# Kernel optimization log

Measured on AMD Instinct MI355X. Metric: run time of the kernel, lower is better.

Reference implementation:

```python
import jax, jax.numpy as jnp
import numpy as np

N_NODES = 50000
N_EDGES = 800000
IN_CH = 128
HID = 256
N_GRAPHS = 512


def setup_inputs() -> dict:
    key = jax.random.key(0)
    ks = jax.random.split(key, 10)
    x = jax.random.normal(ks[0], (N_NODES, IN_CH), dtype=jnp.float32)
    edge_index = jax.random.randint(ks[1], (2, N_EDGES), 0, N_NODES, dtype=jnp.int32)
    batch = jnp.sort(jax.random.randint(ks[2], (N_NODES,), 0, N_GRAPHS, dtype=jnp.int32))
    # GCNConv params (glorot-ish init)
    W0 = jax.random.normal(ks[3], (IN_CH, HID), dtype=jnp.float32) / np.sqrt(IN_CH)
    b0 = jnp.zeros((HID,), dtype=jnp.float32)
    W1 = jax.random.normal(ks[4], (HID, HID), dtype=jnp.float32) / np.sqrt(HID)
    b1 = jnp.zeros((HID,), dtype=jnp.float32)
    W2 = jax.random.normal(ks[5], (HID, HID), dtype=jnp.float32) / np.sqrt(HID)
    b2 = jnp.zeros((HID,), dtype=jnp.float32)
    return {"x": x, "W0": W0, "b0": b0, "W1": W1, "b1": b1, "W2": W2, "b2": b2,
            "edge_index": edge_index, "batch": batch}


def _gcn_norm(edge_index, num_nodes):
    # PyG gcn_norm with add_self_loops=True: A_hat = A + I, norm = D^-1/2 A_hat D^-1/2
    src, dst = edge_index[0], edge_index[1]
    loop = jnp.arange(num_nodes, dtype=src.dtype)
    src = jnp.concatenate([src, loop])
    dst = jnp.concatenate([dst, loop])
    deg = jax.ops.segment_sum(jnp.ones_like(dst, dtype=jnp.float32), dst,
                              num_segments=num_nodes)
    dinv = jnp.where(deg > 0, jax.lax.rsqrt(deg), 0.0)
    norm = dinv[src] * dinv[dst]  # [E + N]
    return src, dst, norm


def _gcn_conv(x, W, b, src, dst, norm, num_nodes):
    h = x @ W                                  # [N, out]
    msg = norm[:, None] * h[src]               # gather + scale, [E+N, out]
    out = jax.ops.segment_sum(msg, dst, num_segments=num_nodes)  # scatter-add
    return out + b


def reference(x, W0, b0, W1, b1, W2, b2, edge_index, batch):
    n = x.shape[0]
    src, dst, norm = _gcn_norm(edge_index, n)  # normalization is layer-independent
    h = jax.nn.relu(_gcn_conv(x, W0, b0, src, dst, norm, n))
    h = jax.nn.relu(_gcn_conv(h, W1, b1, src, dst, norm, n))
    h = jax.nn.relu(_gcn_conv(h, W2, b2, src, dst, norm, n))
    # global_add_pool: segment-sum node features by graph id
    return jax.ops.segment_sum(h, batch, num_segments=N_GRAPHS)
```

## Files before the change

kernel.cpp:

```cpp
#include <hip/hip_runtime.h>

constexpr int NN  = 50000;
constexpr int NE  = 800000;
constexpr int CIN = 128;
constexpr int CH  = 256;
constexpr int NG  = 512;

typedef unsigned short ushort_t;
typedef unsigned int uint_t;

static __device__ __forceinline__ ushort_t f2bf(float f) {
    uint_t u = __float_as_uint(f);
    u += 0x7fffu + ((u >> 16) & 1u);
    return (ushort_t)(u >> 16);
}

__global__ void conv_x_kernel(const float4* __restrict__ x, ushort4* __restrict__ xb, int n4) {
    int i = blockIdx.x * blockDim.x + threadIdx.x;
    if (i >= n4) return;
    float4 v = x[i];
    ushort4 o;
    o.x = f2bf(v.x); o.y = f2bf(v.y); o.z = f2bf(v.z); o.w = f2bf(v.w);
    xb[i] = o;
}

__global__ void conv_wt_kernel(const float* __restrict__ W, ushort_t* __restrict__ Wt, int K, int N) {
    int i = blockIdx.x * blockDim.x + threadIdx.x;
    if (i >= K * N) return;
    int k = i / N, n = i % N;
    Wt[(size_t)n * K + k] = f2bf(W[i]);
}

__global__ void count_kernel(const int* __restrict__ dst, int* __restrict__ cnt, int E) {
    int e = blockIdx.x * blockDim.x + threadIdx.x;
    if (e < E) atomicAdd(&cnt[dst[e]], 1);
}

__global__ __launch_bounds__(256) void scan_bsum_kernel(const int* __restrict__ cnt,
                                                        int* __restrict__ bsum, int n) {
    int i = blockIdx.x * 256 + threadIdx.x;
    int v = (i < n) ? cnt[i] : 0;
    #pragma unroll
    for (int off = 32; off >= 1; off >>= 1) v += __shfl_xor(v, off, 64);
    __shared__ int ws[4];
    if ((threadIdx.x & 63) == 0) ws[threadIdx.x >> 6] = v;
    __syncthreads();
    if (threadIdx.x == 0) bsum[blockIdx.x] = ws[0] + ws[1] + ws[2] + ws[3];
}

__global__ __launch_bounds__(256) void scan_boff_kernel(int* __restrict__ bsum, int nb) {
    int tid = threadIdx.x, lane = tid & 63, wid = tid >> 6;
    int v = (tid < nb) ? bsum[tid] : 0;
    int s = v;
    #pragma unroll
    for (int off = 1; off < 64; off <<= 1) {
        int t = __shfl_up(s, off, 64);
        if (lane >= off) s += t;
    }
    __shared__ int wsum[4];
    if (lane == 63) wsum[wid] = s;
    __syncthreads();
    int wadd = 0;
    #pragma unroll
    for (int w = 0; w < 4; w++) if (w < wid) wadd += wsum[w];
    if (tid < nb) bsum[tid] = wadd + s - v;
}

__global__ __launch_bounds__(256) void scan_final_kernel(const int* __restrict__ cnt,
                                                         const int* __restrict__ boff,
                                                         int* __restrict__ rowptr,
                                                         float* __restrict__ dinv, int n) {
    int tid = threadIdx.x, lane = tid & 63, wid = tid >> 6;
    int i = blockIdx.x * 256 + tid;
    int v = (i < n) ? cnt[i] : 0;
    int s = v;
    #pragma unroll
    for (int off = 1; off < 64; off <<= 1) {
        int t = __shfl_up(s, off, 64);
        if (lane >= off) s += t;
    }
    __shared__ int wsum[4];
    if (lane == 63) wsum[wid] = s;
    __syncthreads();
    int wadd = boff[blockIdx.x];
    #pragma unroll
    for (int w = 0; w < 4; w++) if (w < wid) wadd += wsum[w];
    if (i < n) {
        rowptr[i] = wadd + s - v;
        dinv[i]   = rsqrtf((float)v + 1.0f);
        if (i == n - 1) rowptr[n] = wadd + s;
    }
}

__global__ void scatter_kernel(const int* __restrict__ src, const int* __restrict__ dst,
                               const int* __restrict__ rowptr, int* __restrict__ cursor,
                               const float* __restrict__ dinv, int2* __restrict__ epack, int E) {
    int e = blockIdx.x * blockDim.x + threadIdx.x;
    if (e >= E) return;
    int d = dst[e];
    int s = src[e];
    int p = rowptr[d] + atomicAdd(&cursor[d], 1);
    epack[p] = make_int2(s, __float_as_int(dinv[s]));
}

template <int C, int MODE>
__global__ __launch_bounds__(256) void node_agg_kernel(
    const ushort_t* __restrict__ h, const int* __restrict__ rowptr,
    const int2* __restrict__ epack, const float* __restrict__ dinv,
    const float* __restrict__ bias, const int* __restrict__ batch,
    void* __restrict__ out_v, int n) {
    constexpr int V = C / 64;
    int wave = threadIdx.x >> 6;
    int lane = threadIdx.x & 63;
    int d = blockIdx.x * 4 + wave;
    if (d >= n) return;

    int beg = rowptr[d], end = rowptr[d + 1];
    float acc[V] = {};

    for (int e = beg; e < end; e += 8) {
        int   srcs[8];
        float wts[8];
        #pragma unroll
        for (int u = 0; u < 8; u++) {
            int idx = e + u;
            int2 ep = epack[min(idx, NE - 1)];
            bool a = idx < end;
            srcs[u] = a ? ep.x : d;
            wts[u]  = a ? __int_as_float(ep.y) : 0.0f;
        }
        if constexpr (V == 4) {
            uint_t ra[8], rb[8];
            #pragma unroll
            for (int u = 0; u < 8; u++) {
                const uint_t* row = (const uint_t*)(h + (size_t)srcs[u] * C);
                ra[u] = row[lane];
                rb[u] = row[64 + lane];
            }
            #pragma unroll
            for (int u = 0; u < 8; u++) {
                float w = wts[u];
                acc[0] += w * __uint_as_float(ra[u] << 16);
                acc[1] += w * __uint_as_float(ra[u] & 0xffff0000u);
                acc[2] += w * __uint_as_float(rb[u] << 16);
                acc[3] += w * __uint_as_float(rb[u] & 0xffff0000u);
            }
        } else {
            uint_t rv[8];
            #pragma unroll
            for (int u = 0; u < 8; u++)
                rv[u] = ((const uint_t*)(h + (size_t)srcs[u] * C))[lane];
            #pragma unroll
            for (int u = 0; u < 8; u++) {
                float w = wts[u];
                acc[0] += w * __uint_as_float(rv[u] << 16);
                acc[1] += w * __uint_as_float(rv[u] & 0xffff0000u);
            }
        }
    }

    float dd = dinv[d];
    float self[V];
    {
        const uint_t* row = (const uint_t*)(h + (size_t)d * C);
        uint_t sa = row[lane];
        self[0] = __uint_as_float(sa << 16);
        self[1] = __uint_as_float(sa & 0xffff0000u);
        if constexpr (V == 4) {
            uint_t sb = row[64 + lane];
            self[2] = __uint_as_float(sb << 16);
            self[3] = __uint_as_float(sb & 0xffff0000u);
        }
    }

    float r[V];
    if constexpr (MODE >= 1) {
        float2 bA = *(const float2*)(bias + 2 * lane);
        r[0] = fmaxf(dd * acc[0] + dd * dd * self[0] + bA.x, 0.0f);
        r[1] = fmaxf(dd * acc[1] + dd * dd * self[1] + bA.y, 0.0f);
        if constexpr (V == 4) {
            float2 bB = *(const float2*)(bias + 128 + 2 * lane);
            r[2] = fmaxf(dd * acc[2] + dd * dd * self[2] + bB.x, 0.0f);
            r[3] = fmaxf(dd * acc[3] + dd * dd * self[3] + bB.y, 0.0f);
        }
    } else {
        #pragma unroll
        for (int i = 0; i < V; i++)
            r[i] = dd * acc[i] + dd * dd * self[i];
    }

    if constexpr (MODE == 2) {
        float* o = (float*)out_v + (size_t)batch[d] * C;
        atomicAdd(o + 2 * lane, r[0]);
        atomicAdd(o + 2 * lane + 1, r[1]);
        if constexpr (V == 4) {
            atomicAdd(o + 128 + 2 * lane, r[2]);
            atomicAdd(o + 128 + 2 * lane + 1, r[3]);
        }
    } else {
        uint_t* o = (uint_t*)((ushort_t*)out_v + (size_t)d * C);
        o[lane] = (uint_t)f2bf(r[0]) | ((uint_t)f2bf(r[1]) << 16);
        if constexpr (V == 4)
            o[64 + lane] = (uint_t)f2bf(r[2]) | ((uint_t)f2bf(r[3]) << 16);
    }
}

typedef __attribute__((ext_vector_type(8))) short bf16x8;
typedef __attribute__((ext_vector_type(4))) float f32x4;

template <int MODE>
__global__ __launch_bounds__(256) void gemm_bf16_kernel(
    const ushort_t* __restrict__ A, const ushort_t* __restrict__ Wt,
    const float* __restrict__ bias, ushort_t* __restrict__ C, int M, int K) {
    __shared__ ushort_t As[128][40];
    __shared__ ushort_t Bs[128][40];
    int tid = threadIdx.x;
    int row0 = blockIdx.x * 128, col0 = blockIdx.y * 128;
    int lr = tid >> 2, lq = tid & 3;
    int lane = tid & 63, wv = tid >> 6;
    int wr = (wv >> 1) * 64, wc = (wv & 1) * 64;
    int r16 = lane & 15, quad = lane >> 4;

    f32x4 acc[4][4] = {};

    for (int k0 = 0; k0 < K; k0 += 32) {
        {
            int gr0 = row0 + lr, gr1 = row0 + lr + 64;
            uint4 a0 = make_uint4(0, 0, 0, 0), a1 = make_uint4(0, 0, 0, 0);
            if (gr0 < M) a0 = *(const uint4*)(A + (size_t)gr0 * K + k0 + lq * 8);
            if (gr1 < M) a1 = *(const uint4*)(A + (size_t)gr1 * K + k0 + lq * 8);
            *(uint4*)&As[lr][lq * 8]      = a0;
            *(uint4*)&As[lr + 64][lq * 8] = a1;
            uint4 b0 = *(const uint4*)(Wt + (size_t)(col0 + lr) * K + k0 + lq * 8);
            uint4 b1 = *(const uint4*)(Wt + (size_t)(col0 + lr + 64) * K + k0 + lq * 8);
            *(uint4*)&Bs[lr][lq * 8]      = b0;
            *(uint4*)&Bs[lr + 64][lq * 8] = b1;
        }
        __syncthreads();
        bf16x8 af[4], bfr[4];
        #pragma unroll
        for (int i = 0; i < 4; i++) af[i]  = *(const bf16x8*)&As[wr + i * 16 + r16][quad * 8];
        #pragma unroll
        for (int j = 0; j < 4; j++) bfr[j] = *(const bf16x8*)&Bs[wc + j * 16 + r16][quad * 8];
        #pragma unroll
        for (int i = 0; i < 4; i++)
            #pragma unroll
            for (int j = 0; j < 4; j++)
                acc[i][j] = __builtin_amdgcn_mfma_f32_16x16x32_bf16(af[i], bfr[j], acc[i][j], 0, 0, 0);
        __syncthreads();
    }

    #pragma unroll
    for (int j = 0; j < 4; j++) {
        int colc = col0 + wc + j * 16 + r16;
        float bval = (MODE == 1) ? bias[colc] : 0.0f;
        #pragma unroll
        for (int i = 0; i < 4; i++) {
            #pragma unroll
            for (int r = 0; r < 4; r++) {
                int row = row0 + wr + i * 16 + quad * 4 + r;
                if (row < M) {
                    float v = acc[i][j][r];
                    if (MODE == 1) v = fmaxf(v + bval, 0.0f);
                    C[(size_t)row * 256 + colc] = f2bf(v);
                }
            }
        }
    }
}

extern "C" void kernel_launch(void* const* d_in, const int* in_sizes, int n_in,
                              void* d_out, int out_size, void* d_ws, size_t ws_size,
                              hipStream_t stream) {
    const float* x   = (const float*)d_in[0];
    const float* W0  = (const float*)d_in[1];
    const float* b0  = (const float*)d_in[2];
    const float* W1  = (const float*)d_in[3];
    const float* b1  = (const float*)d_in[4];
    const float* W2  = (const float*)d_in[5];
    const float* b2  = (const float*)d_in[6];
    const int*   ei  = (const int*)d_in[7];
    const int*   src = ei;
    const int*   dst = ei + NE;
    const int*   batch = (const int*)d_in[8];
    float* out = (float*)d_out;

    char* ws = (char*)d_ws;
    ushort_t* Abf = (ushort_t*)ws;
    ushort_t* Bbf = (ushort_t*)(ws + 25600000ull);
    ushort_t* xbf = (ushort_t*)(ws + 51200000ull);
    ushort_t* W0t = (ushort_t*)(ws + 64000000ull);
    ushort_t* W1t = (ushort_t*)(ws + 64065536ull);
    ushort_t* W2t = (ushort_t*)(ws + 64196608ull);
    float*    dinv   = (float*)(ws + 64327680ull);
    int*      rowptr = (int*)  (ws + 64527680ull);
    int*      cnt    = (int*)  (ws + 64727808ull);
    int2*     epack  = (int2*) (ws + 64927808ull);
    int*      bsum   = (int*)  (ws + 71327808ull);

    const int scanBlocks = (NN + 255) / 256;
    const int nodeBlocks = (NN + 3) / 4;
    const dim3 ggrid((NN + 127) / 128, 2);

    conv_x_kernel<<<(NN * CIN / 4 + 255) / 256, 256, 0, stream>>>((const float4*)x, (ushort4*)xbf, NN * CIN / 4);
    conv_wt_kernel<<<(CIN * CH + 255) / 256, 256, 0, stream>>>(W0, W0t, CIN, CH);
    conv_wt_kernel<<<(CH * CH + 255) / 256, 256, 0, stream>>>(W1, W1t, CH, CH);
    conv_wt_kernel<<<(CH * CH + 255) / 256, 256, 0, stream>>>(W2, W2t, CH, CH);

    hipMemsetAsync(cnt, 0, (size_t)NN * 4, stream);
    count_kernel<<<(NE + 255) / 256, 256, 0, stream>>>(dst, cnt, NE);
    scan_bsum_kernel<<<scanBlocks, 256, 0, stream>>>(cnt, bsum, NN);
    scan_boff_kernel<<<1, 256, 0, stream>>>(bsum, scanBlocks);
    scan_final_kernel<<<scanBlocks, 256, 0, stream>>>(cnt, bsum, rowptr, dinv, NN);
    hipMemsetAsync(cnt, 0, (size_t)NN * 4, stream);
    scatter_kernel<<<(NE + 255) / 256, 256, 0, stream>>>(src, dst, rowptr, cnt, dinv, epack, NE);

    node_agg_kernel<CIN, 0><<<nodeBlocks, 256, 0, stream>>>(xbf, rowptr, epack, dinv, nullptr, nullptr, Bbf, NN);
    gemm_bf16_kernel<1><<<ggrid, 256, 0, stream>>>(Bbf, W0t, b0, Abf, NN, CIN);

    gemm_bf16_kernel<0><<<ggrid, 256, 0, stream>>>(Abf, W1t, nullptr, Bbf, NN, CH);
    node_agg_kernel<CH, 1><<<nodeBlocks, 256, 0, stream>>>(Bbf, rowptr, epack, dinv, b1, nullptr, Abf, NN);

    gemm_bf16_kernel<0><<<ggrid, 256, 0, stream>>>(Abf, W2t, nullptr, Bbf, NN, CH);
    hipMemsetAsync(out, 0, (size_t)NG * CH * 4, stream);
    node_agg_kernel<CH, 2><<<nodeBlocks, 256, 0, stream>>>(Bbf, rowptr, epack, dinv, b2, batch, out, NN);
}
```

Before: 457.5 us.

## Slice aggregation by channel chunks and pack edge src/weight into 32 bits

The neighbour-aggregation kernel is restructured so each block covers one of eight channel slices. Several nodes share a wave, with a small lane group per node that loops to the group's maximum degree. The aim is to shrink the gathered working set per slice so feature rows stay in cache, and to make gathers narrower. Edge records are compressed to a 16-bit source id plus an fp16 normalization weight, halving edge-list traffic. In exchange, the edge list is re-read once per slice, lanes idle on low-degree nodes within a group, and the fp16 weight and 16-bit index rely on the node count staying under 65536.

```diff
diff --git a/kernel.cpp b/kernel.cpp
--- a/kernel.cpp
+++ b/kernel.cpp
@@ -1,4 +1,5 @@
 #include <hip/hip_runtime.h>
+#include <hip/hip_fp16.h>
 
 constexpr int NN  = 50000;
 constexpr int NE  = 800000;
@@ -13,6 +14,10 @@
     uint_t u = __float_as_uint(f);
     u += 0x7fffu + ((u >> 16) & 1u);
     return (ushort_t)(u >> 16);
+}
+
+static __device__ __forceinline__ float h16tof(uint_t bits) {
+    return __half2float(__ushort_as_half((unsigned short)bits));
 }
 
 __global__ void conv_x_kernel(const float4* __restrict__ x, ushort4* __restrict__ xb, int n4) {
@@ -94,114 +99,106 @@
 
 __global__ void scatter_kernel(const int* __restrict__ src, const int* __restrict__ dst,
                                const int* __restrict__ rowptr, int* __restrict__ cursor,
-                               const float* __restrict__ dinv, int2* __restrict__ epack, int E) {
+                               const float* __restrict__ dinv, uint_t* __restrict__ epack, int E) {
     int e = blockIdx.x * blockDim.x + threadIdx.x;
     if (e >= E) return;
     int d = dst[e];
     int s = src[e];
     int p = rowptr[d] + atomicAdd(&cursor[d], 1);
-    epack[p] = make_int2(s, __float_as_int(dinv[s]));
+    uint_t hb = (uint_t)__half_as_ushort(__float2half(dinv[s]));
+    epack[p] = (uint_t)s | (hb << 16);
 }
 
 template <int C, int MODE>
 __global__ __launch_bounds__(256) void node_agg_kernel(
     const ushort_t* __restrict__ h, const int* __restrict__ rowptr,
-    const int2* __restrict__ epack, const float* __restrict__ dinv,
+    const uint_t* __restrict__ epack, const float* __restrict__ dinv,
     const float* __restrict__ bias, const int* __restrict__ batch,
     void* __restrict__ out_v, int n) {
-    constexpr int V = C / 64;
-    int wave = threadIdx.x >> 6;
-    int lane = threadIdx.x & 63;
-    int d = blockIdx.x * 4 + wave;
-    if (d >= n) return;
-
-    int beg = rowptr[d], end = rowptr[d + 1];
-    float acc[V] = {};
-
-    for (int e = beg; e < end; e += 8) {
-        int   srcs[8];
-        float wts[8];
+    static_assert(C == 128 || C == 256, "C");
+    constexpr int NPG    = (C == 256) ? 4 : 8;
+    constexpr int GL     = 64 / NPG;
+    constexpr int LOG_GL = (C == 256) ? 4 : 3;
+    constexpr int RS     = C / 2;
+    constexpr int SCH    = 2 * GL;
+
+    int slice = blockIdx.x;
+    int tid  = threadIdx.x;
+    int wave = tid >> 6, lane = tid & 63;
+    int g  = lane >> LOG_GL;
+    int cl = lane & (GL - 1);
+    int d  = (blockIdx.y * 4 + wave) * NPG + g;
+    bool valid = d < n;
+    int ds = valid ? d : 0;
+
+    int beg = rowptr[ds];
+    int end = rowptr[ds + 1];
+    int deg = valid ? (end - beg) : 0;
+
+    int m = deg;
+    #pragma unroll
+    for (int off = GL; off < 64; off <<= 1) {
+        int t = __shfl_xor(m, off, 64);
+        m = max(m, t);
+    }
+
+    const uint_t* hu = (const uint_t*)h;
+    int coff = slice * GL + cl;
+
+    float a0 = 0.0f, a1 = 0.0f;
+    for (int e = 0; e < m; e += 8) {
+        uint_t eps[8];
         #pragma unroll
         for (int u = 0; u < 8; u++) {
-            int idx = e + u;
-            int2 ep = epack[min(idx, NE - 1)];
-            bool a = idx < end;
-            srcs[u] = a ? ep.x : d;
-            wts[u]  = a ? __int_as_float(ep.y) : 0.0f;
-        }
-        if constexpr (V == 4) {
-            uint_t ra[8], rb[8];
-            #pragma unroll
-            for (int u = 0; u < 8; u++) {
-                const uint_t* row = (const uint_t*)(h + (size_t)srcs[u] * C);
-                ra[u] = row[lane];
-                rb[u] = row[64 + lane];
-            }
-            #pragma unroll
-            for (int u = 0; u < 8; u++) {
-                float w = wts[u];
-                acc[0] += w * __uint_as_float(ra[u] << 16);
-                acc[1] += w * __uint_as_float(ra[u] & 0xffff0000u);
-                acc[2] += w * __uint_as_float(rb[u] << 16);
-                acc[3] += w * __uint_as_float(rb[u] & 0xffff0000u);
-            }
-        } else {
-            uint_t rv[8];
-            #pragma unroll
-            for (int u = 0; u < 8; u++)
-                rv[u] = ((const uint_t*)(h + (size_t)srcs[u] * C))[lane];
-            #pragma unroll
-            for (int u = 0; u < 8; u++) {
-                float w = wts[u];
-                acc[0] += w * __uint_as_float(rv[u] << 16);
-                acc[1] += w * __uint_as_float(rv[u] & 0xffff0000u);
-            }
-        }
-    }
-
-    float dd = dinv[d];
-    float self[V];
-    {
-        const uint_t* row = (const uint_t*)(h + (size_t)d * C);
-        uint_t sa = row[lane];
-        self[0] = __uint_as_float(sa << 16);
-        self[1] = __uint_as_float(sa & 0xffff0000u);
-        if constexpr (V == 4) {
-            uint_t sb = row[64 + lane];
-            self[2] = __uint_as_float(sb << 16);
-            self[3] = __uint_as_float(sb & 0xffff0000u);
-        }
-    }
-
-    float r[V];
+            int idx = beg + e + u;
+            eps[u] = epack[min(idx, NE - 1)];
+        }
+        int srcs[8];
+        float ws[8];
+        #pragma unroll
+        for (int u = 0; u < 8; u++) {
+            bool act = (e + u) < deg;
+            srcs[u] = act ? (int)(eps[u] & 0xffffu) : ds;
+            ws[u]   = act ? h16tof(eps[u] >> 16) : 0.0f;
+        }
+        uint_t rv[8];
+        #pragma unroll
+        for (int u = 0; u < 8; u++)
+            rv[u] = hu[srcs[u] * RS + coff];
+        #pragma unroll
+        for (int u = 0; u < 8; u++) {
+            float w = ws[u];
+            a0 += w * __uint_as_float(rv[u] << 16);
+            a1 += w * __uint_as_float(rv[u] & 0xffff0000u);
+        }
+    }
+
+    float dd = dinv[ds];
+    uint_t sv = hu[ds * RS + coff];
+    float s0 = __uint_as_float(sv << 16);
+    float s1 = __uint_as_float(sv & 0xffff0000u);
+
+    float r0, r1;
     if constexpr (MODE >= 1) {
-        float2 bA = *(const float2*)(bias + 2 * lane);
-        r[0] = fmaxf(dd * acc[0] + dd * dd * self[0] + bA.x, 0.0f);
-        r[1] = fmaxf(dd * acc[1] + dd * dd * self[1] + bA.y, 0.0f);
-        if constexpr (V == 4) {
-            float2 bB = *(const float2*)(bias + 128 + 2 * lane);
-            r[2] = fmaxf(dd * acc[2] + dd * dd * self[2] + bB.x, 0.0f);
-            r[3] = fmaxf(dd * acc[3] + dd * dd * self[3] + bB.y, 0.0f);
-        }
+        float2 b2 = *(const float2*)(bias + slice * SCH + 2 * cl);
+        r0 = fmaxf(dd * a0 + dd * dd * s0 + b2.x, 0.0f);
+        r1 = fmaxf(dd * a1 + dd * dd * s1 + b2.y, 0.0f);
     } else {
-        #pragma unroll
-        for (int i = 0; i < V; i++)
-            r[i] = dd * acc[i] + dd * dd * self[i];
+        r0 = dd * a0 + dd * dd * s0;
+        r1 = dd * a1 + dd * dd * s1;
     }
 
     if constexpr (MODE == 2) {
-        float* o = (float*)out_v + (size_t)batch[d] * C;
-        atomicAdd(o + 2 * lane, r[0]);
-        atomicAdd(o + 2 * lane + 1, r[1]);
-        if constexpr (V == 4) {
-            atomicAdd(o + 128 + 2 * lane, r[2]);
-            atomicAdd(o + 128 + 2 * lane + 1, r[3]);
+        if (valid) {
+            float* o = (float*)out_v + (size_t)batch[ds] * C + slice * SCH + 2 * cl;
+            atomicAdd(o, r0);
+            atomicAdd(o + 1, r1);
         }
     } else {
-        uint_t* o = (uint_t*)((ushort_t*)out_v + (size_t)d * C);
-        o[lane] = (uint_t)f2bf(r[0]) | ((uint_t)f2bf(r[1]) << 16);
-        if constexpr (V == 4)
-            o[64 + lane] = (uint_t)f2bf(r[2]) | ((uint_t)f2bf(r[3]) << 16);
+        if (valid) {
+            uint_t* o = (uint_t*)out_v;
+            o[d * RS + coff] = (uint_t)f2bf(r0) | ((uint_t)f2bf(r1) << 16);
+        }
     }
 }
 
@@ -295,12 +292,13 @@
     float*    dinv   = (float*)(ws + 64327680ull);
     int*      rowptr = (int*)  (ws + 64527680ull);
     int*      cnt    = (int*)  (ws + 64727808ull);
-    int2*     epack  = (int2*) (ws + 64927808ull);
+    uint_t*   epack  = (uint_t*)(ws + 64927808ull);
     int*      bsum   = (int*)  (ws + 71327808ull);
 
     const int scanBlocks = (NN + 255) / 256;
-    const int nodeBlocks = (NN + 3) / 4;
     const dim3 ggrid((NN + 127) / 128, 2);
+    const dim3 agrid256(8, (NN + 15) / 16);
+    const dim3 agrid128(8, (NN + 31) / 32);
 
     conv_x_kernel<<<(NN * CIN / 4 + 255) / 256, 256, 0, stream>>>((const float4*)x, (ushort4*)xbf, NN * CIN / 4);
     conv_wt_kernel<<<(CIN * CH + 255) / 256, 256, 0, stream>>>(W0, W0t, CIN, CH);
@@ -315,13 +313,13 @@
     hipMemsetAsync(cnt, 0, (size_t)NN * 4, stream);
     scatter_kernel<<<(NE + 255) / 256, 256, 0, stream>>>(src, dst, rowptr, cnt, dinv, epack, NE);
 
-    node_agg_kernel<CIN, 0><<<nodeBlocks, 256, 0, stream>>>(xbf, rowptr, epack, dinv, nullptr, nullptr, Bbf, NN);
+    node_agg_kernel<CIN, 0><<<agrid128, 256, 0, stream>>>(xbf, rowptr, epack, dinv, nullptr, nullptr, Bbf, NN);
     gemm_bf16_kernel<1><<<ggrid, 256, 0, stream>>>(Bbf, W0t, b0, Abf, NN, CIN);
 
     gemm_bf16_kernel<0><<<ggrid, 256, 0, stream>>>(Abf, W1t, nullptr, Bbf, NN, CH);
-    node_agg_kernel<CH, 1><<<nodeBlocks, 256, 0, stream>>>(Bbf, rowptr, epack, dinv, b1, nullptr, Abf, NN);
+    node_agg_kernel<CH, 1><<<agrid256, 256, 0, stream>>>(Bbf, rowptr, epack, dinv, b1, nullptr, Abf, NN);
 
     gemm_bf16_kernel<0><<<ggrid, 256, 0, stream>>>(Abf, W2t, nullptr, Bbf, NN, CH);
     hipMemsetAsync(out, 0, (size_t)NG * CH * 4, stream);
-    node_agg_kernel<CH, 2><<<nodeBlocks, 256, 0, stream>>>(Bbf, rowptr, epack, dinv, b2, batch, out, NN);
-}
+    node_agg_kernel<CH, 2><<<agrid256, 256, 0, stream>>>(Bbf, rowptr, epack, dinv, b2, batch, out, NN);
+}
```

After: 669.5 us. 1.46x slower.

## Pack CSR edges into 32-bit words with padded rows and prefetched vector loads

Applied to the files above, without the earlier changes.

Each edge entry now packs a 16-bit source index and an fp16 source normalisation into one 32-bit word. CSR rows are padded to a multiple of 8 so each group of eight edges is fetched with two aligned uint4 loads, and the next group is prefetched. The per-node degree is read separately, and row and source indices are made wave-uniform with readfirstlane so row addressing happens on the scalar unit. The aim is to cut edge-list bandwidth and per-edge load instructions in the three aggregation kernels. The cost is lower precision on edge weights (fp16) and a 16-bit index limit that only works because the node count is below 65536.

```diff
diff --git a/kernel.cpp b/kernel.cpp
--- a/kernel.cpp
+++ b/kernel.cpp
@@ -1,4 +1,5 @@
 #include <hip/hip_runtime.h>
+#include <hip/hip_fp16.h>
 
 constexpr int NN  = 50000;
 constexpr int NE  = 800000;
@@ -13,6 +14,10 @@
     uint_t u = __float_as_uint(f);
     u += 0x7fffu + ((u >> 16) & 1u);
     return (ushort_t)(u >> 16);
+}
+
+static __device__ __forceinline__ float h16tof(uint_t bits) {
+    return __half2float(__ushort_as_half((unsigned short)bits));
 }
 
 __global__ void conv_x_kernel(const float4* __restrict__ x, ushort4* __restrict__ xb, int n4) {
@@ -39,7 +44,7 @@
 __global__ __launch_bounds__(256) void scan_bsum_kernel(const int* __restrict__ cnt,
                                                         int* __restrict__ bsum, int n) {
     int i = blockIdx.x * 256 + threadIdx.x;
-    int v = (i < n) ? cnt[i] : 0;
+    int v = (i < n) ? ((cnt[i] + 7) & ~7) : 0;
     #pragma unroll
     for (int off = 32; off >= 1; off >>= 1) v += __shfl_xor(v, off, 64);
     __shared__ int ws[4];
@@ -72,7 +77,8 @@
                                                          float* __restrict__ dinv, int n) {
     int tid = threadIdx.x, lane = tid & 63, wid = tid >> 6;
     int i = blockIdx.x * 256 + tid;
-    int v = (i < n) ? cnt[i] : 0;
+    int c = (i < n) ? cnt[i] : 0;
+    int v = (c + 7) & ~7;
     int s = v;
     #pragma unroll
     for (int off = 1; off < 64; off <<= 1) {
@@ -87,53 +93,61 @@
     for (int w = 0; w < 4; w++) if (w < wid) wadd += wsum[w];
     if (i < n) {
         rowptr[i] = wadd + s - v;
-        dinv[i]   = rsqrtf((float)v + 1.0f);
+        dinv[i]   = rsqrtf((float)c + 1.0f);
         if (i == n - 1) rowptr[n] = wadd + s;
     }
 }
 
 __global__ void scatter_kernel(const int* __restrict__ src, const int* __restrict__ dst,
                                const int* __restrict__ rowptr, int* __restrict__ cursor,
-                               const float* __restrict__ dinv, int2* __restrict__ epack, int E) {
+                               const float* __restrict__ dinv, uint_t* __restrict__ epack, int E) {
     int e = blockIdx.x * blockDim.x + threadIdx.x;
     if (e >= E) return;
     int d = dst[e];
     int s = src[e];
     int p = rowptr[d] + atomicAdd(&cursor[d], 1);
-    epack[p] = make_int2(s, __float_as_int(dinv[s]));
+    uint_t hb = (uint_t)__half_as_ushort(__float2half(dinv[s]));
+    epack[p] = (uint_t)s | (hb << 16);
 }
 
 template <int C, int MODE>
 __global__ __launch_bounds__(256) void node_agg_kernel(
     const ushort_t* __restrict__ h, const int* __restrict__ rowptr,
-    const int2* __restrict__ epack, const float* __restrict__ dinv,
-    const float* __restrict__ bias, const int* __restrict__ batch,
-    void* __restrict__ out_v, int n) {
+    const int* __restrict__ degc, const uint_t* __restrict__ epack,
+    const float* __restrict__ dinv, const float* __restrict__ bias,
+    const int* __restrict__ batch, void* __restrict__ out_v, int n) {
     constexpr int V = C / 64;
     int wave = threadIdx.x >> 6;
     int lane = threadIdx.x & 63;
     int d = blockIdx.x * 4 + wave;
     if (d >= n) return;
 
-    int beg = rowptr[d], end = rowptr[d + 1];
+    int beg = __builtin_amdgcn_readfirstlane(rowptr[d]);
+    int deg = __builtin_amdgcn_readfirstlane(degc[d]);
+    const uint_t* hu = (const uint_t*)h;
+
     float acc[V] = {};
-
-    for (int e = beg; e < end; e += 8) {
+    const uint4* ep4 = (const uint4*)(epack + beg);
+    uint4 ea, eb, na, nb;
+    if (deg > 0) { ea = ep4[0]; eb = ep4[1]; }
+
+    for (int e = 0; e < deg; e += 8) {
+        int blk = e >> 3;
+        if (e + 8 < deg) { na = ep4[blk * 2 + 2]; nb = ep4[blk * 2 + 3]; }
+        uint_t eps[8] = {ea.x, ea.y, ea.z, ea.w, eb.x, eb.y, eb.z, eb.w};
         int   srcs[8];
         float wts[8];
         #pragma unroll
         for (int u = 0; u < 8; u++) {
-            int idx = e + u;
-            int2 ep = epack[min(idx, NE - 1)];
-            bool a = idx < end;
-            srcs[u] = a ? ep.x : d;
-            wts[u]  = a ? __int_as_float(ep.y) : 0.0f;
+            bool a = (e + u) < deg;
+            srcs[u] = a ? (int)(eps[u] & 0xffffu) : d;
+            wts[u]  = a ? h16tof(eps[u] >> 16) : 0.0f;
         }
         if constexpr (V == 4) {
             uint_t ra[8], rb[8];
             #pragma unroll
             for (int u = 0; u < 8; u++) {
-                const uint_t* row = (const uint_t*)(h + (size_t)srcs[u] * C);
+                const uint_t* row = hu + (size_t)__builtin_amdgcn_readfirstlane(srcs[u]) * (C / 2);
                 ra[u] = row[lane];
                 rb[u] = row[64 + lane];
             }
@@ -148,8 +162,10 @@
         } else {
             uint_t rv[8];
             #pragma unroll
-            for (int u = 0; u < 8; u++)
-                rv[u] = ((const uint_t*)(h + (size_t)srcs[u] * C))[lane];
+            for (int u = 0; u < 8; u++) {
+                const uint_t* row = hu + (size_t)__builtin_amdgcn_readfirstlane(srcs[u]) * (C / 2);
+                rv[u] = row[lane];
+            }
             #pragma unroll
             for (int u = 0; u < 8; u++) {
                 float w = wts[u];
@@ -157,12 +173,13 @@
                 acc[1] += w * __uint_as_float(rv[u] & 0xffff0000u);
             }
         }
+        ea = na; eb = nb;
     }
 
     float dd = dinv[d];
     float self[V];
     {
-        const uint_t* row = (const uint_t*)(h + (size_t)d * C);
+        const uint_t* row = hu + (size_t)d * (C / 2);
         uint_t sa = row[lane];
         self[0] = __uint_as_float(sa << 16);
         self[1] = __uint_as_float(sa & 0xffff0000u);
@@ -295,8 +312,9 @@
     float*    dinv   = (float*)(ws + 64327680ull);
     int*      rowptr = (int*)  (ws + 64527680ull);
     int*      cnt    = (int*)  (ws + 64727808ull);
-    int2*     epack  = (int2*) (ws + 64927808ull);
+    uint_t*   epack  = (uint_t*)(ws + 64927808ull);
     int*      bsum   = (int*)  (ws + 71327808ull);
+    int*      cursor = (int*)ws;
 
     const int scanBlocks = (NN + 255) / 256;
     const int nodeBlocks = (NN + 3) / 4;
@@ -312,16 +330,16 @@
     scan_bsum_kernel<<<scanBlocks, 256, 0, stream>>>(cnt, bsum, NN);
     scan_boff_kernel<<<1, 256, 0, stream>>>(bsum, scanBlocks);
     scan_final_kernel<<<scanBlocks, 256, 0, stream>>>(cnt, bsum, rowptr, dinv, NN);
-    hipMemsetAsync(cnt, 0, (size_t)NN * 4, stream);
-    scatter_kernel<<<(NE + 255) / 256, 256, 0, stream>>>(src, dst, rowptr, cnt, dinv, epack, NE);
-
-    node_agg_kernel<CIN, 0><<<nodeBlocks, 256, 0, stream>>>(xbf, rowptr, epack, dinv, nullptr, nullptr, Bbf, NN);
+    hipMemsetAsync(cursor, 0, (size_t)NN * 4, stream);
+    scatter_kernel<<<(NE + 255) / 256, 256, 0, stream>>>(src, dst, rowptr, cursor, dinv, epack, NE);
+
+    node_agg_kernel<CIN, 0><<<nodeBlocks, 256, 0, stream>>>(xbf, rowptr, cnt, epack, dinv, nullptr, nullptr, Bbf, NN);
     gemm_bf16_kernel<1><<<ggrid, 256, 0, stream>>>(Bbf, W0t, b0, Abf, NN, CIN);
 
     gemm_bf16_kernel<0><<<ggrid, 256, 0, stream>>>(Abf, W1t, nullptr, Bbf, NN, CH);
-    node_agg_kernel<CH, 1><<<nodeBlocks, 256, 0, stream>>>(Bbf, rowptr, epack, dinv, b1, nullptr, Abf, NN);
+    node_agg_kernel<CH, 1><<<nodeBlocks, 256, 0, stream>>>(Bbf, rowptr, cnt, epack, dinv, b1, nullptr, Abf, NN);
 
     gemm_bf16_kernel<0><<<ggrid, 256, 0, stream>>>(Abf, W2t, nullptr, Bbf, NN, CH);
     hipMemsetAsync(out, 0, (size_t)NG * CH * 4, stream);
-    node_agg_kernel<CH, 2><<<nodeBlocks, 256, 0, stream>>>(Bbf, rowptr, epack, dinv, b2, batch, out, NN);
-}
+    node_agg_kernel<CH, 2><<<nodeBlocks, 256, 0, stream>>>(Bbf, rowptr, cnt, epack, dinv, b2, batch, out, NN);
+}
```

New measurement: 442.1 us. -3.4%, faster.
